# Kernel optimization log

Measured on AMD Instinct MI355X. Metric: run time of the kernel, lower is better.

## Reference

```python
import jax, jax.numpy as jnp
import numpy as np

DIM, NH, WS, SR, CTS = 256, 8, 8, 4, 2
HD = DIM // NH
SCALE = HD ** -0.5

def _linear(x, w, b=None):
    y = x @ w.T
    return y + b if b is not None else y

def _ln(x, g, b, eps=1e-5):
    m = jnp.mean(x, -1, keepdims=True)
    v = jnp.mean((x - m) ** 2, -1, keepdims=True)
    return (x - m) / jnp.sqrt(v + eps) * g + b

def _mlp(x, w1, b1, w2, b2):
    return _linear(jax.nn.gelu(_linear(x, w1, b1), approximate=False), w2, b2)

def _pos_emb_rank3(seq_len, w1, b1, w2):
    # PosEmbMLPSwinv1D with rank=3: coords on cube_root(seq) grid, normalized
    s = int(round(seq_len ** (1.0 / 3.0)))
    c = (jnp.arange(s, dtype=jnp.float32) - s // 2) / (s // 2)
    grid = jnp.stack(jnp.meshgrid(c, c, c, indexing='ij'))      # (3,s,s,s)
    tbl = grid.reshape(3, -1).T                                 # (s^3,3)
    return _linear(jax.nn.relu(_linear(tbl, w1, b1)), w2)[None]  # (1,s^3,dim)

def _rel_bias_3d(ws, w1, b1, w2, n_global):
    # PosEmbMLPSwinv3D: CPB-MLP bias over 3D relative coords, 16*sigmoid, zero-pad for carrier tokens
    r = jnp.arange(-(ws - 1), ws, dtype=jnp.float32)
    tbl = jnp.stack(jnp.meshgrid(r, r, r, indexing='ij'), axis=-1) / (ws - 1)
    tbl = tbl * 8.0
    tbl = jnp.sign(tbl) * jnp.log2(jnp.abs(tbl) + 1.0) / np.log2(8.0)
    table = _linear(jax.nn.relu(_linear(tbl.reshape(-1, 3), w1, b1)), w2)  # ((2ws-1)^3, NH)
    coords = jnp.stack(jnp.meshgrid(jnp.arange(ws), jnp.arange(ws), jnp.arange(ws), indexing='ij'))
    cf = coords.reshape(3, -1)
    rel = (cf[:, :, None] - cf[:, None, :]).transpose(1, 2, 0) + (ws - 1)  # (P,P,3)
    idx = rel[..., 0] * (2 * ws - 1) ** 2 + rel[..., 1] * (2 * ws - 1) + rel[..., 2]
    P = ws ** 3
    bias = table[idx.reshape(-1)].reshape(P, P, NH).transpose(2, 0, 1)
    bias = 16.0 * jax.nn.sigmoid(bias)
    return jnp.pad(bias, ((0, 0), (n_global, 0), (n_global, 0)))[None]  # (1,NH,P+g,P+g)

def _win_attn(x, qkv_w, qkv_b, proj_w, proj_b, bias):
    B, N, C = x.shape
    qkv = _linear(x, qkv_w, qkv_b).reshape(B, N, 3, NH, HD).transpose(2, 0, 3, 1, 4)
    q, k, v = qkv[0], qkv[1], qkv[2]
    attn = jax.nn.softmax(jnp.einsum('bhnd,bhmd->bhnm', q, k) * SCALE + bias, axis=-1)
    out = jnp.einsum('bhnm,bhmd->bhnd', attn, v).transpose(0, 2, 1, 3).reshape(B, N, C)
    return _linear(out, proj_w, proj_b)

def _ct_dewindow(ct, W, H, D, ws):
    bs, _, N = ct.shape
    c = ct.reshape(bs, W // ws, H // ws, D // ws, ws, ws, ws, N)
    c = c.transpose(0, 7, 1, 3, 5, 2, 4, 6).reshape(bs, N, W * H * D)
    return c.transpose(0, 2, 1)

def _ct_window(ct, W, H, D, ws):
    bs, _, N = ct.shape
    c = ct.reshape(bs, H // ws, ws, W // ws, ws, D // ws, ws, N)
    return c.transpose(0, 1, 3, 5, 2, 4, 6, 7)

def setup_inputs() -> dict:
    key = jax.random.key(0)
    ks = jax.random.split(key, 48)
    B0 = 1
    nw = SR ** 3
    def w(k, *s):
        return jax.random.normal(k, s, jnp.float32) * 0.02
    def b(k, *s):
        return jax.random.normal(k, s, jnp.float32) * 0.01
    d4 = 4 * DIM
    return {
        'x': jax.random.normal(ks[0], (B0 * nw, WS ** 3, DIM), jnp.float32),
        'ct': jax.random.normal(ks[1], (B0, (CTS * SR) ** 3, DIM), jnp.float32),
        'pe_w1': w(ks[2], 512, 3), 'pe_b1': b(ks[3], 512), 'pe_w2': w(ks[4], DIM, 512),
        'hpe_w1': w(ks[5], 512, 3), 'hpe_b1': b(ks[6], 512), 'hpe_w2': w(ks[7], DIM, 512),
        'hat_n1_g': jnp.ones((DIM,), jnp.float32), 'hat_n1_b': jnp.zeros((DIM,), jnp.float32),
        'hat_qkv_w': w(ks[8], 3 * DIM, DIM), 'hat_qkv_b': b(ks[9], 3 * DIM),
        'hat_proj_w': w(ks[10], DIM, DIM), 'hat_proj_b': b(ks[11], DIM),
        'hat_cpb_w1': w(ks[12], 512, 3), 'hat_cpb_b1': b(ks[13], 512), 'hat_cpb_w2': w(ks[14], NH, 512),
        'hat_n2_g': jnp.ones((DIM,), jnp.float32), 'hat_n2_b': jnp.zeros((DIM,), jnp.float32),
        'hat_fc1_w': w(ks[15], d4, DIM), 'hat_fc1_b': b(ks[16], d4),
        'hat_fc2_w': w(ks[17], DIM, d4), 'hat_fc2_b': b(ks[18], DIM),
        'n1_g': jnp.ones((DIM,), jnp.float32), 'n1_b': jnp.zeros((DIM,), jnp.float32),
        'qkv_w': w(ks[19], 3 * DIM, DIM), 'qkv_b': b(ks[20], 3 * DIM),
        'proj_w': w(ks[21], DIM, DIM), 'proj_b': b(ks[22], DIM),
        'cpb_w1': w(ks[23], 512, 3), 'cpb_b1': b(ks[24], 512), 'cpb_w2': w(ks[25], NH, 512),
        'n2_g': jnp.ones((DIM,), jnp.float32), 'n2_b': jnp.zeros((DIM,), jnp.float32),
        'fc1_w': w(ks[26], d4, DIM), 'fc1_b': b(ks[27], d4),
        'fc2_w': w(ks[28], DIM, d4), 'fc2_b': b(ks[29], DIM),
    }

def reference(x, ct, pe_w1, pe_b1, pe_w2, hpe_w1, hpe_b1, hpe_w2,
              hat_n1_g, hat_n1_b, hat_qkv_w, hat_qkv_b, hat_proj_w, hat_proj_b,
              hat_cpb_w1, hat_cpb_b1, hat_cpb_w2, hat_n2_g, hat_n2_b,
              hat_fc1_w, hat_fc1_b, hat_fc2_w, hat_fc2_b,
              n1_g, n1_b, qkv_w, qkv_b, proj_w, proj_b,
              cpb_w1, cpb_b1, cpb_w2, n2_g, n2_b, fc1_w, fc1_b, fc2_w, fc2_b):
    Bg, Ng, Hg = ct.shape
    G = CTS * SR  # carrier-token global cube side
    x = x + _pos_emb_rank3(x.shape[1], pe_w1, pe_b1, pe_w2)
    # carrier-token global attention (hierarchical path)
    ct = _ct_dewindow(ct, G, G, G, CTS)
    ct = ct + _pos_emb_rank3(ct.shape[1], hpe_w1, hpe_b1, hpe_w2)
    hat_bias = _rel_bias_3d(G, hat_cpb_w1, hat_cpb_b1, hat_cpb_w2, 0)
    ct = ct + _win_attn(_ln(ct, hat_n1_g, hat_n1_b), hat_qkv_w, hat_qkv_b, hat_proj_w, hat_proj_b, hat_bias)
    ct = ct + _mlp(_ln(ct, hat_n2_g, hat_n2_b), hat_fc1_w, hat_fc1_b, hat_fc2_w, hat_fc2_b)
    ct_w = _ct_window(ct, G, G, G, CTS).reshape(x.shape[0], -1, Hg)
    # windowed attention over [carrier tokens ; window tokens]
    x = jnp.concatenate([ct_w, x], axis=1)
    bias = _rel_bias_3d(WS, cpb_w1, cpb_b1, cpb_w2, CTS ** 3)
    x = x + _win_attn(_ln(x, n1_g, n1_b), qkv_w, qkv_b, proj_w, proj_b, bias)
    x = x + _mlp(_ln(x, n2_g, n2_b), fc1_w, fc1_b, fc2_w, fc2_b)
    split = x.shape[1] - WS ** 3
    ctr, x = x[:, :split], x[:, split:]
    return x, ctr.reshape(Bg, Ng, Hg)
```

## Files before the change

### kernel.cpp

```cpp
#include <hip/hip_runtime.h>
#include <hip/hip_bf16.h>
#include <math.h>

typedef __hip_bfloat16 bf16;

#define SCALE_QK 0.17677669529663687f

__device__ __forceinline__ float b2f(bf16 v){ return __bfloat162float(v); }
__device__ __forceinline__ bf16  f2b(float v){ return __float2bfloat16(v); }
__device__ __forceinline__ short bfs(float x){ bf16 b = f2b(x); short s; __builtin_memcpy(&s, &b, 2); return s; }

struct __align__(16) bf16x8 { bf16 v[8]; };
struct __align__(8)  bf16x4 { bf16 v[4]; };

typedef __attribute__((ext_vector_type(8))) short sh8;
typedef __attribute__((ext_vector_type(4))) short sh4;
typedef __attribute__((ext_vector_type(4))) float f4;

#if defined(__has_builtin)
#if __has_builtin(__builtin_amdgcn_mfma_f32_16x16x16bf16_1k)
#define HAS_MFMA16 1
#else
#define HAS_MFMA16 0
#endif
#else
#define HAS_MFMA16 0
#endif

#if defined(__has_builtin)
#if __has_builtin(__builtin_amdgcn_exp2f)
#define EXP2(x) __builtin_amdgcn_exp2f(x)
#else
#define EXP2(x) exp2f(x)
#endif
#else
#define EXP2(x) exp2f(x)
#endif

__device__ __forceinline__ void gl16(const bf16* g, short* l) {
    __builtin_amdgcn_global_load_lds((const __attribute__((address_space(1))) void*)g,
                                     (__attribute__((address_space(3))) void*)l, 16, 0, 0);
}

__global__ __launch_bounds__(256) void wcvt10_k(const float* s0, const float* s1, const float* s2, const float* s3,
                                                const float* s4, const float* s5, const float* s6, const float* s7,
                                                const float* s8, const float* s9,
                                                bf16* d0, bf16* d1, bf16* d2, bf16* d3, bf16* d4,
                                                bf16* d5, bf16* d6, bf16* d7, bf16* d8, bf16* d9) {
    const int sizes[10] = {196608, 65536, 262144, 262144, 196608, 65536, 262144, 262144, 131072, 131072};
    int which = blockIdx.y;
    const float* s; bf16* d;
    switch (which) {
        case 0: s = s0; d = d0; break;  case 1: s = s1; d = d1; break;
        case 2: s = s2; d = d2; break;  case 3: s = s3; d = d3; break;
        case 4: s = s4; d = d4; break;  case 5: s = s5; d = d5; break;
        case 6: s = s6; d = d6; break;  case 7: s = s7; d = d7; break;
        case 8: s = s8; d = d8; break;  default: s = s9; d = d9; break;
    }
    int i = blockIdx.x * 256 + threadIdx.x;
    if (i < sizes[which]) d[i] = f2b(s[i]);
}

__global__ __launch_bounds__(256) void hidbuild_k(const float* __restrict__ w1a, const float* __restrict__ b1a,
                                                  const float* __restrict__ w1b, const float* __restrict__ b1b,
                                                  bf16* __restrict__ hidA, bf16* __restrict__ hidB) {
    const float* w1 = blockIdx.y ? w1b : w1a;
    const float* b1 = blockIdx.y ? b1b : b1a;
    bf16* hid       = blockIdx.y ? hidB : hidA;
    int t = blockIdx.x, tid = threadIdx.x;
    int i = t >> 6, j = (t >> 3) & 7, k = t & 7;
    float c0 = (i - 4) * 0.25f, c1 = (j - 4) * 0.25f, c2 = (k - 4) * 0.25f;
    #pragma unroll
    for (int rep = 0; rep < 2; rep++) {
        int jj = tid + rep * 256;
        float h = c0 * w1[jj*3+0] + c1 * w1[jj*3+1] + c2 * w1[jj*3+2] + b1[jj];
        hid[(size_t)t * 512 + jj] = f2b(fmaxf(h, 0.f));
    }
}

__device__ __forceinline__ float cpb_coord(int idx) {
    float v = (idx - 7) * (8.0f / 7.0f);
    return copysignf(log2f(fabsf(v) + 1.0f) * (1.0f / 3.0f), v);
}
__global__ __launch_bounds__(512) void cpbtab_k(const float* __restrict__ w1a, const float* __restrict__ b1a,
                                                const float* __restrict__ w2a, float* __restrict__ taba,
                                                const float* __restrict__ w1b, const float* __restrict__ b1b,
                                                const float* __restrict__ w2b, float* __restrict__ tabb) {
    const float* w1 = blockIdx.y ? w1b : w1a;
    const float* b1 = blockIdx.y ? b1b : b1a;
    const float* w2 = blockIdx.y ? w2b : w2a;
    float* tab      = blockIdx.y ? tabb : taba;
    int t = blockIdx.x, tid = threadIdx.x;
    __shared__ float hid[512];
    int i = t / 225, r = t - i * 225, j = r / 15, k = r - j * 15;
    float x0 = cpb_coord(i), x1 = cpb_coord(j), x2 = cpb_coord(k);
    float h = x0 * w1[tid*3+0] + x1 * w1[tid*3+1] + x2 * w1[tid*3+2] + b1[tid];
    hid[tid] = fmaxf(h, 0.f);
    __syncthreads();
    int h8 = tid >> 6, lane = tid & 63;
    float p = 0.f;
    for (int jj = lane; jj < 512; jj += 64) p += hid[jj] * w2[h8*512 + jj];
    for (int off = 32; off; off >>= 1) p += __shfl_down(p, off);
    if (lane == 0) tab[t * 8 + h8] = p;
}

__global__ __launch_bounds__(256) void biasbuild_k(const float* __restrict__ taba, float* __restrict__ biasQa,
                                                   const float* __restrict__ tabb, float* __restrict__ biasQb) {
    const float* tab = blockIdx.y ? tabb : taba;
    float* biasQ     = blockIdx.y ? biasQb : biasQa;
    int idx = blockIdx.x * 256 + threadIdx.x;
    int h = idx >> 18, rem = idx & 262143;
    int q = rem >> 9, k = rem & 511;
    int qx = q >> 6, qy = (q >> 3) & 7, qz = q & 7;
    int kx = k >> 6, ky = (k >> 3) & 7, kz = k & 7;
    int tidx = ((qx - kx + 7) * 15 + (qy - ky + 7)) * 15 + (qz - kz + 7);
    float v = tab[tidx * 8 + h];
    float b = 16.f / (1.f + __expf(-v));
    biasQ[idx] = (b - 24.0f) * 1.4426950408889634f;
}

__global__ __launch_bounds__(256) void ct0ln_k(const float* __restrict__ ct_in,
                                               const float* __restrict__ hpe,
                                               const float* __restrict__ g,
                                               const float* __restrict__ b,
                                               float* __restrict__ ct0,
                                               bf16* __restrict__ lnout) {
    int u = blockIdx.x, c = threadIdx.x;
    int a = u >> 7, cc = (u >> 5) & 3, e = (u >> 4) & 1, bb = (u >> 2) & 3, d = (u >> 1) & 1, f = u & 1;
    int t = a * 128 + bb * 32 + cc * 8 + d * 4 + e * 2 + f;
    float x = ct_in[(size_t)t * 256 + c] + hpe[(size_t)u * 256 + c];
    ct0[(size_t)u * 256 + c] = x;
    float s = x, s2 = x * x;
    for (int off = 32; off; off >>= 1) { s += __shfl_down(s, off); s2 += __shfl_down(s2, off); }
    __shared__ float red[8];
    int wid = c >> 6, lane = c & 63;
    if (lane == 0) { red[wid] = s; red[wid + 4] = s2; }
    __syncthreads();
    if (c == 0) { red[0] = red[0] + red[1] + red[2] + red[3]; red[4] = red[4] + red[5] + red[6] + red[7]; }
    __syncthreads();
    float mean = red[0] * (1.f / 256.f);
    float var  = fmaxf(red[4] * (1.f / 256.f) - mean * mean, 0.f);
    float rstd = rsqrtf(var + 1e-5f);
    lnout[(size_t)u * 256 + c] = f2b((x - mean) * rstd * g[c] + b[c]);
}

__global__ __launch_bounds__(256) void ln_k(const float* __restrict__ in,
                                            const float* __restrict__ g,
                                            const float* __restrict__ b,
                                            bf16* __restrict__ out) {
    int row = blockIdx.x, c = threadIdx.x;
    float x = in[(size_t)row * 256 + c];
    float s = x, s2 = x * x;
    for (int off = 32; off; off >>= 1) { s += __shfl_down(s, off); s2 += __shfl_down(s2, off); }
    __shared__ float red[8];
    int wid = c >> 6, lane = c & 63;
    if (lane == 0) { red[wid] = s; red[wid + 4] = s2; }
    __syncthreads();
    if (c == 0) { red[0] = red[0] + red[1] + red[2] + red[3]; red[4] = red[4] + red[5] + red[6] + red[7]; }
    __syncthreads();
    float mean = red[0] * (1.f / 256.f);
    float var  = fmaxf(red[4] * (1.f / 256.f) - mean * mean, 0.f);
    float rstd = rsqrtf(var + 1e-5f);
    out[(size_t)row * 256 + c] = f2b((x - mean) * rstd * g[c] + b[c]);
}

template <int MODE>
__global__ __launch_bounds__(256) void gemm_k(const bf16* __restrict__ A,
                                              const bf16* __restrict__ W,
                                              const float* __restrict__ bias,
                                              int M, int N, int K,
                                              float* __restrict__ res,
                                              bf16* __restrict__ outb) {
    __shared__ short As[2][128 * 32];
    __shared__ short Ws[2][128 * 32];
    int m0 = blockIdx.y * 128, n0 = blockIdx.x * 128;
    int tid = threadIdx.x;
    int lane = tid & 63, wave = tid >> 6;
    int quad = lane >> 4, m16 = lane & 15;
    int wm = (wave & 1) * 64, wn = (wave >> 1) * 64;
    int arow = tid >> 2, acol = (tid & 3) * 8;

    const bf16* Ab = A + (size_t)(m0 + arow) * K + acol;
    const bf16* A2 = Ab + (size_t)64 * K;
    const bf16* Wb = W + (size_t)(n0 + arow) * K + acol;
    const bf16* W2 = Wb + (size_t)64 * K;

    f4 acc[4][4];
    #pragma unroll
    for (int i = 0; i < 4; i++)
        #pragma unroll
        for (int j = 0; j < 4; j++) acc[i][j] = (f4){0.f, 0.f, 0.f, 0.f};

    gl16(Ab, &As[0][tid * 8]);
    gl16(A2, &As[0][2048 + tid * 8]);
    gl16(Wb, &Ws[0][tid * 8]);
    gl16(W2, &Ws[0][2048 + tid * 8]);

    int cur = 0;
    for (int k0 = 0; k0 < K; k0 += 32) {
        int nxt = cur ^ 1;
        if (k0 + 32 < K) {
            gl16(Ab + k0 + 32, &As[nxt][tid * 8]);
            gl16(A2 + k0 + 32, &As[nxt][2048 + tid * 8]);
            gl16(Wb + k0 + 32, &Ws[nxt][tid * 8]);
            gl16(W2 + k0 + 32, &Ws[nxt][2048 + tid * 8]);
            asm volatile("s_waitcnt vmcnt(4)" ::: "memory");
        } else {
            asm volatile("s_waitcnt vmcnt(0)" ::: "memory");
        }
        __builtin_amdgcn_s_barrier();
        sh8 af[4], bf[4];
        #pragma unroll
        for (int mi = 0; mi < 4; mi++)
            af[mi] = *reinterpret_cast<const sh8*>(&As[cur][(wm + mi * 16 + m16) * 32 + quad * 8]);
        #pragma unroll
        for (int ni = 0; ni < 4; ni++)
            bf[ni] = *reinterpret_cast<const sh8*>(&Ws[cur][(wn + ni * 16 + m16) * 32 + quad * 8]);
        #pragma unroll
        for (int mi = 0; mi < 4; mi++)
            #pragma unroll
            for (int ni = 0; ni < 4; ni++)
                acc[mi][ni] = __builtin_amdgcn_mfma_f32_16x16x32_bf16(af[mi], bf[ni], acc[mi][ni], 0, 0, 0);
        __builtin_amdgcn_s_barrier();
        cur = nxt;
    }
    (void)M;

    #pragma unroll
    for (int mi = 0; mi < 4; mi++) {
        #pragma unroll
        for (int r = 0; r < 4; r++) {
            int gm = m0 + wm + mi * 16 + quad * 4 + r;
            #pragma unroll
            for (int ni = 0; ni < 4; ni++) {
                int gn = n0 + wn + ni * 16 + m16;
                float v = acc[mi][ni][r];
                if constexpr (MODE != 3) v += bias[gn];
                if constexpr (MODE == 2)      res[(size_t)gm * N + gn] += v;
                else if constexpr (MODE == 3) res[(size_t)gm * N + gn] = v;
                else if constexpr (MODE == 1) outb[(size_t)gm * N + gn] = f2b(0.5f * v * (1.0f + erff(v * 0.70710678118654752f)));
                else                          outb[(size_t)gm * N + gn] = f2b(v);
            }
        }
    }
}

__global__ __launch_bounds__(512) void gemmln_k(const bf16* __restrict__ A,
                                                const bf16* __restrict__ W,
                                                const float* __restrict__ bias,
                                                float* __restrict__ xcat,
                                                const float* __restrict__ g,
                                                const float* __restrict__ b,
                                                bf16* __restrict__ outb) {
    __shared__ short As[2][128 * 32];
    __shared__ short Ws[2][256 * 32];
    __shared__ float redS[128 * 4];
    __shared__ float redQ[128 * 4];
    __shared__ float stat[128 * 2];
    int m0 = blockIdx.x * 128;
    int tid = threadIdx.x;
    int lane = tid & 63, wave = tid >> 6;
    int quad = lane >> 4, m16 = lane & 15;
    int wm = (wave >> 2) * 64, wn = (wave & 3) * 64;
    int arow = tid >> 2, acol = (tid & 3) * 8;

    const bf16* Ab = A + (size_t)(m0 + arow) * 256 + acol;
    const bf16* Wb = W + (size_t)arow * 256 + acol;
    const bf16* W2 = Wb + (size_t)128 * 256;

    f4 acc[4][4];
    #pragma unroll
    for (int i = 0; i < 4; i++)
        #pragma unroll
        for (int j = 0; j < 4; j++) acc[i][j] = (f4){0.f, 0.f, 0.f, 0.f};

    gl16(Ab, &As[0][tid * 8]);
    gl16(Wb, &Ws[0][tid * 8]);
    gl16(W2, &Ws[0][4096 + tid * 8]);

    int cur = 0;
    for (int k0 = 0; k0 < 256; k0 += 32) {
        int nxt = cur ^ 1;
        if (k0 + 32 < 256) {
            gl16(Ab + k0 + 32, &As[nxt][tid * 8]);
            gl16(Wb + k0 + 32, &Ws[nxt][tid * 8]);
            gl16(W2 + k0 + 32, &Ws[nxt][4096 + tid * 8]);
            asm volatile("s_waitcnt vmcnt(3)" ::: "memory");
        } else {
            asm volatile("s_waitcnt vmcnt(0)" ::: "memory");
        }
        __builtin_amdgcn_s_barrier();
        sh8 af[4], bf[4];
        #pragma unroll
        for (int mi = 0; mi < 4; mi++)
            af[mi] = *reinterpret_cast<const sh8*>(&As[cur][(wm + mi * 16 + m16) * 32 + quad * 8]);
        #pragma unroll
        for (int ni = 0; ni < 4; ni++)
            bf[ni] = *reinterpret_cast<const sh8*>(&Ws[cur][(wn + ni * 16 + m16) * 32 + quad * 8]);
        #pragma unroll
        for (int mi = 0; mi < 4; mi++)
            #pragma unroll
            for (int ni = 0; ni < 4; ni++)
                acc[mi][ni] = __builtin_amdgcn_mfma_f32_16x16x32_bf16(af[mi], bf[ni], acc[mi][ni], 0, 0, 0);
        __builtin_amdgcn_s_barrier();
        cur = nxt;
    }

    #pragma unroll
    for (int mi = 0; mi < 4; mi++) {
        #pragma unroll
        for (int r = 0; r < 4; r++) {
            int lr = wm + mi * 16 + quad * 4 + r;
            int gm = m0 + lr;
            float ps = 0.f, pq = 0.f;
            #pragma unroll
            for (int ni = 0; ni < 4; ni++) {
                int gc = wn + ni * 16 + m16;
                float v = acc[mi][ni][r] + bias[gc] + xcat[(size_t)gm * 256 + gc];
                acc[mi][ni][r] = v;
                ps += v; pq += v * v;
            }
            ps += __shfl_xor(ps, 1); pq += __shfl_xor(pq, 1);
            ps += __shfl_xor(ps, 2); pq += __shfl_xor(pq, 2);
            ps += __shfl_xor(ps, 4); pq += __shfl_xor(pq, 4);
            ps += __shfl_xor(ps, 8); pq += __shfl_xor(pq, 8);
            if (m16 == 0) { redS[lr * 4 + (wave & 3)] = ps; redQ[lr * 4 + (wave & 3)] = pq; }
        }
    }
    __syncthreads();
    if (tid < 128) {
        float s = redS[tid * 4] + redS[tid * 4 + 1] + redS[tid * 4 + 2] + redS[tid * 4 + 3];
        float q = redQ[tid * 4] + redQ[tid * 4 + 1] + redQ[tid * 4 + 2] + redQ[tid * 4 + 3];
        float mean = s * (1.f / 256.f);
        float var  = fmaxf(q * (1.f / 256.f) - mean * mean, 0.f);
        stat[tid * 2]     = mean;
        stat[tid * 2 + 1] = rsqrtf(var + 1e-5f);
    }
    __syncthreads();
    #pragma unroll
    for (int mi = 0; mi < 4; mi++) {
        #pragma unroll
        for (int r = 0; r < 4; r++) {
            int lr = wm + mi * 16 + quad * 4 + r;
            int gm = m0 + lr;
            float mean = stat[lr * 2], rstd = stat[lr * 2 + 1];
            #pragma unroll
            for (int ni = 0; ni < 4; ni++) {
                int gc = wn + ni * 16 + m16;
                float v = acc[mi][ni][r];
                xcat[(size_t)gm * 256 + gc] = v;
                outb[(size_t)gm * 256 + gc] = f2b((v - mean) * rstd * g[gc] + b[gc]);
            }
        }
    }
}

__global__ __launch_bounds__(256) void gemmsplit_k(const bf16* __restrict__ A,
                                                   const bf16* __restrict__ W,
                                                   const float* __restrict__ bias,
                                                   int K,
                                                   const float* __restrict__ res,
                                                   float* __restrict__ out) {
    __shared__ short As[2][128 * 32];
    __shared__ short Ws[2][128 * 32];
    int m0 = blockIdx.y * 128, n0 = blockIdx.x * 128;
    int tid = threadIdx.x;
    int lane = tid & 63, wave = tid >> 6;
    int quad = lane >> 4, m16 = lane & 15;
    int wm = (wave & 1) * 64, wn = (wave >> 1) * 64;
    int arow = tid >> 2, acol = (tid & 3) * 8;

    const bf16* Ab = A + (size_t)(m0 + arow) * K + acol;
    const bf16* A2 = Ab + (size_t)64 * K;
    const bf16* Wb = W + (size_t)(n0 + arow) * K + acol;
    const bf16* W2 = Wb + (size_t)64 * K;

    f4 acc[4][4];
    #pragma unroll
    for (int i = 0; i < 4; i++)
        #pragma unroll
        for (int j = 0; j < 4; j++) acc[i][j] = (f4){0.f, 0.f, 0.f, 0.f};

    gl16(Ab, &As[0][tid * 8]);
    gl16(A2, &As[0][2048 + tid * 8]);
    gl16(Wb, &Ws[0][tid * 8]);
    gl16(W2, &Ws[0][2048 + tid * 8]);

    int cur = 0;
    for (int k0 = 0; k0 < K; k0 += 32) {
        int nxt = cur ^ 1;
        if (k0 + 32 < K) {
            gl16(Ab + k0 + 32, &As[nxt][tid * 8]);
            gl16(A2 + k0 + 32, &As[nxt][2048 + tid * 8]);
            gl16(Wb + k0 + 32, &Ws[nxt][tid * 8]);
            gl16(W2 + k0 + 32, &Ws[nxt][2048 + tid * 8]);
            asm volatile("s_waitcnt vmcnt(4)" ::: "memory");
        } else {
            asm volatile("s_waitcnt vmcnt(0)" ::: "memory");
        }
        __builtin_amdgcn_s_barrier();
        sh8 af[4], bf[4];
        #pragma unroll
        for (int mi = 0; mi < 4; mi++)
            af[mi] = *reinterpret_cast<const sh8*>(&As[cur][(wm + mi * 16 + m16) * 32 + quad * 8]);
        #pragma unroll
        for (int ni = 0; ni < 4; ni++)
            bf[ni] = *reinterpret_cast<const sh8*>(&Ws[cur][(wn + ni * 16 + m16) * 32 + quad * 8]);
        #pragma unroll
        for (int mi = 0; mi < 4; mi++)
            #pragma unroll
            for (int ni = 0; ni < 4; ni++)
                acc[mi][ni] = __builtin_amdgcn_mfma_f32_16x16x32_bf16(af[mi], bf[ni], acc[mi][ni], 0, 0, 0);
        __builtin_amdgcn_s_barrier();
        cur = nxt;
    }

    #pragma unroll
    for (int mi = 0; mi < 4; mi++) {
        #pragma unroll
        for (int r = 0; r < 4; r++) {
            int gm = m0 + wm + mi * 16 + quad * 4 + r;
            int w = gm / 520, p = gm - w * 520;
            size_t drow = (p >= 8) ? (size_t)(w * 512 + p - 8) : (size_t)(32768 + w * 8 + p);
            #pragma unroll
            for (int ni = 0; ni < 4; ni++) {
                int gn = n0 + wn + ni * 16 + m16;
                float v = acc[mi][ni][r] + bias[gn] + res[(size_t)gm * 256 + gn];
                out[drow * 256 + gn] = v;
            }
        }
    }
}

#define VSTR 548
#define SC2   0.25503575360579045f
#define CNB  (-34.62468098133512f)
#define NEGB (-1.0e30f)
__device__ __forceinline__ f4 bias_ld(const float* brow, bool vq, int tg, int N, int glob) {
    if (tg >= N) return (f4){NEGB, NEGB, NEGB, NEGB};
    if (vq && tg >= glob) return *reinterpret_cast<const f4*>(brow + tg);
    return (f4){CNB, CNB, CNB, CNB};
}
__global__ __launch_bounds__(512) void flash_k(const bf16* __restrict__ qkv,
                                               const float* __restrict__ biasQ,
                                               bf16* __restrict__ out,
                                               int N, int glob) {
    int wh = blockIdx.x, w = wh >> 3, h = wh & 7;
    int qs = blockIdx.y;
    int tid = threadIdx.x;
    int lane = tid & 63, wave = tid >> 6;
    int quad = lane >> 4, qcol = lane & 15;
    const int NT32 = (N + 31) & ~31;

    __shared__ __align__(16) char smem[32 * VSTR * 2];
    bf16* Vt = reinterpret_cast<bf16*>(smem);
#if !HAS_MFMA16
    __shared__ float Ps[8][16 * 17];
#endif

    for (int i = tid; i < NT32 * 4; i += 512) {
        int tok = i >> 2, seg = i & 3;
        if (tok < N) {
            const bf16* vp = qkv + ((size_t)(w * N + tok)) * 768 + 512 + h * 32 + seg * 8;
            bf16x8 vv = *reinterpret_cast<const bf16x8*>(vp);
            #pragma unroll
            for (int e = 0; e < 8; e++) Vt[(seg * 8 + e) * VSTR + tok] = vv.v[e];
        } else {
            bf16 z = f2b(0.f);
            #pragma unroll
            for (int e = 0; e < 8; e++) Vt[(seg * 8 + e) * VSTR + tok] = z;
        }
    }
    __syncthreads();

    const bf16* qbase = qkv + ((size_t)w * N) * 768 + h * 32;
    const bf16* kbase = qbase + 256;
    int nqt = (N + 15) >> 4, nkt = NT32 >> 5;
    int nfull = nqt >> 1;

    if (qs < 2) {
        int u = wave + 8 * qs;
        if (u < nfull) {
            int qA = u * 32 + qcol;
            int qB = qA + 16;
            sh8 qfA = *reinterpret_cast<const sh8*>(qbase + (size_t)qA * 768 + quad * 8);
            sh8 qfB = *reinterpret_cast<const sh8*>(qbase + (size_t)qB * 768 + quad * 8);
            f4 O0A = {0.f,0.f,0.f,0.f}, O1A = {0.f,0.f,0.f,0.f};
            f4 O0B = {0.f,0.f,0.f,0.f}, O1B = {0.f,0.f,0.f,0.f};
            float lA = 0.f, lB = 0.f;
            bool vA = (qA >= glob);
            bool vB = (qB >= glob);
            const float* browA = biasQ + (((size_t)h << 9) + (size_t)(vA ? (qA - glob) : 0)) * 512 - glob;
            const float* browB = biasQ + (((size_t)h << 9) + (size_t)(vB ? (qB - glob) : 0)) * 512 - glob;

            sh8 kf0, kf1;
            f4 nb0A, nb1A, nb0B, nb1B;
            {
                int k0 = qcol, k1 = 16 + qcol;
                kf0 = *reinterpret_cast<const sh8*>(kbase + (size_t)((k0 < N) ? k0 : (N - 1)) * 768 + quad * 8);
                kf1 = *reinterpret_cast<const sh8*>(kbase + (size_t)((k1 < N) ? k1 : (N - 1)) * 768 + quad * 8);
                int tg0 = quad * 4, tg1 = 16 + quad * 4;
                nb0A = bias_ld(browA, vA, tg0, N, glob);
                nb1A = bias_ld(browA, vA, tg1, N, glob);
                nb0B = bias_ld(browB, vB, tg0, N, glob);
                nb1B = bias_ld(browB, vB, tg1, N, glob);
            }

            for (int kt = 0; kt < nkt; kt++) {
                int bt = kt * 32;
                sh8 c0 = kf0, c1 = kf1;
                f4 bb0A = nb0A, bb1A = nb1A, bb0B = nb0B, bb1B = nb1B;
                if (kt + 1 < nkt) {
                    int btn = bt + 32;
                    int n0 = btn + qcol, n1 = btn + 16 + qcol;
                    kf0 = *reinterpret_cast<const sh8*>(kbase + (size_t)((n0 < N) ? n0 : (N - 1)) * 768 + quad * 8);
                    kf1 = *reinterpret_cast<const sh8*>(kbase + (size_t)((n1 < N) ? n1 : (N - 1)) * 768 + quad * 8);
                    int tg0n = btn + quad * 4, tg1n = btn + 16 + quad * 4;
                    nb0A = bias_ld(browA, vA, tg0n, N, glob);
                    nb1A = bias_ld(browA, vA, tg1n, N, glob);
                    nb0B = bias_ld(browB, vB, tg0n, N, glob);
                    nb1B = bias_ld(browB, vB, tg1n, N, glob);
                }
                f4 z = {0.f, 0.f, 0.f, 0.f};
                f4 s0A = __builtin_amdgcn_mfma_f32_16x16x32_bf16(c0, qfA, z, 0, 0, 0);
                f4 s1A = __builtin_amdgcn_mfma_f32_16x16x32_bf16(c1, qfA, z, 0, 0, 0);
                f4 s0B = __builtin_amdgcn_mfma_f32_16x16x32_bf16(c0, qfB, z, 0, 0, 0);
                f4 s1B = __builtin_amdgcn_mfma_f32_16x16x32_bf16(c1, qfB, z, 0, 0, 0);

                float pA[8], pB[8];
                #pragma unroll
                for (int r = 0; r < 4; r++) {
                    pA[r]     = EXP2(fmaf(s0A[r], SC2, bb0A[r]));
                    pA[4 + r] = EXP2(fmaf(s1A[r], SC2, bb1A[r]));
                    pB[r]     = EXP2(fmaf(s0B[r], SC2, bb0B[r]));
                    pB[4 + r] = EXP2(fmaf(s1B[r], SC2, bb1B[r]));
                }
                #pragma unroll
                for (int r = 0; r < 8; r++) { lA += pA[r]; lB += pB[r]; }

#if HAS_MFMA16
                sh4 v00 = *reinterpret_cast<const sh4*>(&Vt[qcol * VSTR + bt + quad * 4]);
                sh4 v10 = *reinterpret_cast<const sh4*>(&Vt[qcol * VSTR + bt + 16 + quad * 4]);
                sh4 v01 = *reinterpret_cast<const sh4*>(&Vt[(qcol + 16) * VSTR + bt + quad * 4]);
                sh4 v11 = *reinterpret_cast<const sh4*>(&Vt[(qcol + 16) * VSTR + bt + 16 + quad * 4]);
                sh4 pf0A, pf1A, pf0B, pf1B;
                #pragma unroll
                for (int r = 0; r < 4; r++) {
                    pf0A[r] = bfs(pA[r]); pf1A[r] = bfs(pA[4 + r]);
                    pf0B[r] = bfs(pB[r]); pf1B[r] = bfs(pB[4 + r]);
                }
                O0A = __builtin_amdgcn_mfma_f32_16x16x16bf16_1k(v00, pf0A, O0A, 0, 0, 0);
                O0A = __builtin_amdgcn_mfma_f32_16x16x16bf16_1k(v10, pf1A, O0A, 0, 0, 0);
                O1A = __builtin_amdgcn_mfma_f32_16x16x16bf16_1k(v01, pf0A, O1A, 0, 0, 0);
                O1A = __builtin_amdgcn_mfma_f32_16x16x16bf16_1k(v11, pf1A, O1A, 0, 0, 0);
                O0B = __builtin_amdgcn_mfma_f32_16x16x16bf16_1k(v00, pf0B, O0B, 0, 0, 0);
                O0B = __builtin_amdgcn_mfma_f32_16x16x16bf16_1k(v10, pf1B, O0B, 0, 0, 0);
                O1B = __builtin_amdgcn_mfma_f32_16x16x16bf16_1k(v01, pf0B, O1B, 0, 0, 0);
                O1B = __builtin_amdgcn_mfma_f32_16x16x16bf16_1k(v11, pf1B, O1B, 0, 0, 0);
#else
                for (int t = 0; t < 2; t++) {
                    const float* ph = t ? pB : pA;
                    for (int half = 0; half < 2; half++) {
                        #pragma unroll
                        for (int r = 0; r < 4; r++) Ps[wave][(quad * 4 + r) * 17 + qcol] = ph[half * 4 + r];
                        __builtin_amdgcn_wave_barrier();
                        sh8 pbig, va, vb;
                        #pragma unroll
                        for (int j = 0; j < 8; j++) {
                            int tl = quad * 8 + j;
                            float pv = (quad < 2) ? Ps[wave][tl * 17 + qcol] : 0.f;
                            pbig[j] = bfs(pv);
                            bf16 a0 = (quad < 2) ? Vt[qcol * VSTR + bt + half * 16 + tl] : f2b(0.f);
                            bf16 a1 = (quad < 2) ? Vt[(qcol + 16) * VSTR + bt + half * 16 + tl] : f2b(0.f);
                            short t0, t1;
                            __builtin_memcpy(&t0, &a0, 2); __builtin_memcpy(&t1, &a1, 2);
                            va[j] = t0; vb[j] = t1;
                        }
                        if (t == 0) {
                            O0A = __builtin_amdgcn_mfma_f32_16x16x32_bf16(va, pbig, O0A, 0, 0, 0);
                            O1A = __builtin_amdgcn_mfma_f32_16x16x32_bf16(vb, pbig, O1A, 0, 0, 0);
                        } else {
                            O0B = __builtin_amdgcn_mfma_f32_16x16x32_bf16(va, pbig, O0B, 0, 0, 0);
                            O1B = __builtin_amdgcn_mfma_f32_16x16x32_bf16(vb, pbig, O1B, 0, 0, 0);
                        }
                        __builtin_amdgcn_wave_barrier();
                    }
                }
#endif
            }

            lA += __shfl_xor(lA, 16); lA += __shfl_xor(lA, 32);
            lB += __shfl_xor(lB, 16); lB += __shfl_xor(lB, 32);
            float rlA = 1.f / lA, rlB = 1.f / lB;
            {
                bf16x4 o0, o1;
                #pragma unroll
                for (int r = 0; r < 4; r++) { o0.v[r] = f2b(O0A[r] * rlA); o1.v[r] = f2b(O1A[r] * rlA); }
                bf16* op = out + ((size_t)(w * N + qA)) * 256 + h * 32 + quad * 4;
                *reinterpret_cast<bf16x4*>(op)      = o0;
                *reinterpret_cast<bf16x4*>(op + 16) = o1;
            }
            {
                bf16x4 o0, o1;
                #pragma unroll
                for (int r = 0; r < 4; r++) { o0.v[r] = f2b(O0B[r] * rlB); o1.v[r] = f2b(O1B[r] * rlB); }
                bf16* op = out + ((size_t)(w * N + qB)) * 256 + h * 32 + quad * 4;
                *reinterpret_cast<bf16x4*>(op)      = o0;
                *reinterpret_cast<bf16x4*>(op + 16) = o1;
            }
        }
    } else {
        int rt = nqt - 1;
        int qA = rt * 16 + qcol;
        int qrA = (qA < N) ? qA : (N - 1);
        sh8 qfA = *reinterpret_cast<const sh8*>(qbase + (size_t)qrA * 768 + quad * 8);
        f4 O0 = {0.f,0.f,0.f,0.f}, O1 = {0.f,0.f,0.f,0.f};
        float l = 0.f;
        bool vA = (qA >= glob) && (qA < N);
        const float* browA = biasQ + (((size_t)h << 9) + (size_t)(vA ? (qA - glob) : 0)) * 512 - glob;

        for (int kt = wave; kt < nkt; kt += 8) {
            int bt = kt * 32;
            int k0 = bt + qcol, k1 = bt + 16 + qcol;
            sh8 c0 = *reinterpret_cast<const sh8*>(kbase + (size_t)((k0 < N) ? k0 : (N - 1)) * 768 + quad * 8);
            sh8 c1 = *reinterpret_cast<const sh8*>(kbase + (size_t)((k1 < N) ? k1 : (N - 1)) * 768 + quad * 8);
            f4 z = {0.f, 0.f, 0.f, 0.f};
            f4 s0 = __builtin_amdgcn_mfma_f32_16x16x32_bf16(c0, qfA, z, 0, 0, 0);
            f4 s1 = __builtin_amdgcn_mfma_f32_16x16x32_bf16(c1, qfA, z, 0, 0, 0);

            int tg0 = bt + quad * 4, tg1 = bt + 16 + quad * 4;
            f4 bb0 = bias_ld(browA, vA, tg0, N, glob);
            f4 bb1 = bias_ld(browA, vA, tg1, N, glob);

            float p[8];
            #pragma unroll
            for (int r = 0; r < 4; r++) {
                p[r]     = EXP2(fmaf(s0[r], SC2, bb0[r]));
                p[4 + r] = EXP2(fmaf(s1[r], SC2, bb1[r]));
            }
            #pragma unroll
            for (int r = 0; r < 8; r++) l += p[r];

#if HAS_MFMA16
            sh4 v00 = *reinterpret_cast<const sh4*>(&Vt[qcol * VSTR + bt + quad * 4]);
            sh4 v10 = *reinterpret_cast<const sh4*>(&Vt[qcol * VSTR + bt + 16 + quad * 4]);
            sh4 v01 = *reinterpret_cast<const sh4*>(&Vt[(qcol + 16) * VSTR + bt + quad * 4]);
            sh4 v11 = *reinterpret_cast<const sh4*>(&Vt[(qcol + 16) * VSTR + bt + 16 + quad * 4]);
            sh4 pf0, pf1;
            #pragma unroll
            for (int r = 0; r < 4; r++) { pf0[r] = bfs(p[r]); pf1[r] = bfs(p[4 + r]); }
            O0 = __builtin_amdgcn_mfma_f32_16x16x16bf16_1k(v00, pf0, O0, 0, 0, 0);
            O0 = __builtin_amdgcn_mfma_f32_16x16x16bf16_1k(v10, pf1, O0, 0, 0, 0);
            O1 = __builtin_amdgcn_mfma_f32_16x16x16bf16_1k(v01, pf0, O1, 0, 0, 0);
            O1 = __builtin_amdgcn_mfma_f32_16x16x16bf16_1k(v11, pf1, O1, 0, 0, 0);
#else
            for (int half = 0; half < 2; half++) {
                #pragma unroll
                for (int r = 0; r < 4; r++) Ps[wave][(quad * 4 + r) * 17 + qcol] = p[half * 4 + r];
                __builtin_amdgcn_wave_barrier();
                sh8 pbig, va, vb;
                #pragma unroll
                for (int j = 0; j < 8; j++) {
                    int tl = quad * 8 + j;
                    float pv = (quad < 2) ? Ps[wave][tl * 17 + qcol] : 0.f;
                    pbig[j] = bfs(pv);
                    bf16 a0 = (quad < 2) ? Vt[qcol * VSTR + bt + half * 16 + tl] : f2b(0.f);
                    bf16 a1 = (quad < 2) ? Vt[(qcol + 16) * VSTR + bt + half * 16 + tl] : f2b(0.f);
                    short t0, t1;
                    __builtin_memcpy(&t0, &a0, 2); __builtin_memcpy(&t1, &a1, 2);
                    va[j] = t0; vb[j] = t1;
                }
                O0 = __builtin_amdgcn_mfma_f32_16x16x32_bf16(va, pbig, O0, 0, 0, 0);
                O1 = __builtin_amdgcn_mfma_f32_16x16x32_bf16(vb, pbig, O1, 0, 0, 0);
                __builtin_amdgcn_wave_barrier();
            }
#endif
        }

        __syncthreads();
        float (*red)[64][9] = reinterpret_cast<float (*)[64][9]>(smem);
        #pragma unroll
        for (int r = 0; r < 4; r++) { red[wave][lane][r] = O0[r]; red[wave][lane][4 + r] = O1[r]; }
        red[wave][lane][8] = l;
        __syncthreads();

        if (wave == 0) {
            f4 O0s = {0.f,0.f,0.f,0.f}, O1s = {0.f,0.f,0.f,0.f};
            float ls = 0.f;
            for (int v = 0; v < 8; v++) {
                #pragma unroll
                for (int r = 0; r < 4; r++) { O0s[r] += red[v][lane][r]; O1s[r] += red[v][lane][4 + r]; }
                ls += red[v][lane][8];
            }
            ls += __shfl_xor(ls, 16); ls += __shfl_xor(ls, 32);
            float rl = 1.f / ls;
            if (qA < N) {
                bf16x4 o0, o1;
                #pragma unroll
                for (int r = 0; r < 4; r++) { o0.v[r] = f2b(O0s[r] * rl); o1.v[r] = f2b(O1s[r] * rl); }
                bf16* op = out + ((size_t)(w * N + qA)) * 256 + h * 32 + quad * 4;
                *reinterpret_cast<bf16x4*>(op)      = o0;
                *reinterpret_cast<bf16x4*>(op + 16) = o1;
            }
        }
    }
}

__global__ __launch_bounds__(256) void xcatln_k(const float* __restrict__ x_in,
                                                const float* __restrict__ pe,
                                                const float* __restrict__ ct2,
                                                const float* __restrict__ g,
                                                const float* __restrict__ b,
                                                float* __restrict__ xcat,
                                                bf16* __restrict__ xln) {
    int row = blockIdx.x, w = row / 520, p = row - w * 520, c = threadIdx.x;
    float v;
    if (p < 8) {
        int P = w >> 4, Q = (w >> 2) & 3, R = w & 3;
        int S = p >> 2, T = (p >> 1) & 1, U = p & 1;
        int t = P * 128 + S * 64 + Q * 16 + T * 8 + R * 2 + U;
        v = ct2[(size_t)t * 256 + c];
    } else {
        int t = p - 8;
        v = x_in[((size_t)w * 512 + t) * 256 + c] + pe[(size_t)t * 256 + c];
    }
    xcat[(size_t)row * 256 + c] = v;
    float s = v, s2 = v * v;
    for (int off = 32; off; off >>= 1) { s += __shfl_down(s, off); s2 += __shfl_down(s2, off); }
    __shared__ float red[8];
    int wid = c >> 6, lane = c & 63;
    if (lane == 0) { red[wid] = s; red[wid + 4] = s2; }
    __syncthreads();
    if (c == 0) { red[0] = red[0] + red[1] + red[2] + red[3]; red[4] = red[4] + red[5] + red[6] + red[7]; }
    __syncthreads();
    float mean = red[0] * (1.f / 256.f);
    float var  = fmaxf(red[4] * (1.f / 256.f) - mean * mean, 0.f);
    float rstd = rsqrtf(var + 1e-5f);
    xln[(size_t)row * 256 + c] = f2b((v - mean) * rstd * g[c] + b[c]);
}

__global__ __launch_bounds__(256) void xcatbuild_k(const float* __restrict__ x_in,
                                                   const float* __restrict__ pe,
                                                   const float* __restrict__ ct2,
                                                   float* __restrict__ xcat) {
    int row = blockIdx.x, w = row / 520, p = row - w * 520, c = threadIdx.x;
    float v;
    if (p < 8) {
        int P = w >> 4, Q = (w >> 2) & 3, R = w & 3;
        int S = p >> 2, T = (p >> 1) & 1, U = p & 1;
        int t = P * 128 + S * 64 + Q * 16 + T * 8 + R * 2 + U;
        v = ct2[(size_t)t * 256 + c];
    } else {
        int t = p - 8;
        v = x_in[((size_t)w * 512 + t) * 256 + c] + pe[(size_t)t * 256 + c];
    }
    xcat[(size_t)row * 256 + c] = v;
}

__global__ __launch_bounds__(256) void outbuild_k(const float* __restrict__ xcat,
                                                  float* __restrict__ out) {
    int row = blockIdx.x, w = row / 520, p = row - w * 520, c = threadIdx.x;
    float v = xcat[(size_t)row * 256 + c];
    if (p >= 8) out[((size_t)(w * 512) + (p - 8)) * 256 + c] = v;
    else        out[(size_t)8388608 + ((size_t)(w * 8) + p) * 256 + c] = v;
}

extern "C" void kernel_launch(void* const* d_in, const int* in_sizes, int n_in,
                              void* d_out, int out_size, void* d_ws, size_t ws_size,
                              hipStream_t stream) {
    const float* x          = (const float*)d_in[0];
    const float* ct         = (const float*)d_in[1];
    const float* pe_w1      = (const float*)d_in[2];
    const float* pe_b1      = (const float*)d_in[3];
    const float* pe_w2      = (const float*)d_in[4];
    const float* hpe_w1     = (const float*)d_in[5];
    const float* hpe_b1     = (const float*)d_in[6];
    const float* hpe_w2     = (const float*)d_in[7];
    const float* hat_n1_g   = (const float*)d_in[8];
    const float* hat_n1_b   = (const float*)d_in[9];
    const float* hat_qkv_w  = (const float*)d_in[10];
    const float* hat_qkv_b  = (const float*)d_in[11];
    const float* hat_proj_w = (const float*)d_in[12];
    const float* hat_proj_b = (const float*)d_in[13];
    const float* hat_cpb_w1 = (const float*)d_in[14];
    const float* hat_cpb_b1 = (const float*)d_in[15];
    const float* hat_cpb_w2 = (const float*)d_in[16];
    const float* hat_n2_g   = (const float*)d_in[17];
    const float* hat_n2_b   = (const float*)d_in[18];
    const float* hat_fc1_w  = (const float*)d_in[19];
    const float* hat_fc1_b  = (const float*)d_in[20];
    const float* hat_fc2_w  = (const float*)d_in[21];
    const float* hat_fc2_b  = (const float*)d_in[22];
    const float* n1_g       = (const float*)d_in[23];
    const float* n1_b       = (const float*)d_in[24];
    const float* qkv_w      = (const float*)d_in[25];
    const float* qkv_b      = (const float*)d_in[26];
    const float* proj_w     = (const float*)d_in[27];
    const float* proj_b     = (const float*)d_in[28];
    const float* cpb_w1     = (const float*)d_in[29];
    const float* cpb_b1     = (const float*)d_in[30];
    const float* cpb_w2     = (const float*)d_in[31];
    const float* n2_g       = (const float*)d_in[32];
    const float* n2_b       = (const float*)d_in[33];
    const float* fc1_w      = (const float*)d_in[34];
    const float* fc1_b      = (const float*)d_in[35];
    const float* fc2_w      = (const float*)d_in[36];
    const float* fc2_b      = (const float*)d_in[37];
    (void)in_sizes; (void)n_in; (void)out_size;

    char* base = (char*)d_ws;
    size_t off = 0;
    auto alloc = [&](size_t bytes) -> void* {
        void* p = base + off;
        off += (bytes + 255) & ~(size_t)255;
        return p;
    };
    float* pe        = (float*)alloc(512 * 256 * 4);
    float* hpe       = (float*)alloc(512 * 256 * 4);
    float* tab_hat   = (float*)alloc(3375 * 8 * 4);
    float* tab2      = (float*)alloc(3375 * 8 * 4);
    float* biasQ2    = (float*)alloc((size_t)8 * 512 * 512 * 4);
    float* ct0       = (float*)alloc(512 * 256 * 4);
    bf16* wb_hqkv  = (bf16*)alloc(768 * 256 * 2);
    bf16* wb_hproj = (bf16*)alloc(256 * 256 * 2);
    bf16* wb_hfc1  = (bf16*)alloc(1024 * 256 * 2);
    bf16* wb_hfc2  = (bf16*)alloc(256 * 1024 * 2);
    bf16* wb_qkv   = (bf16*)alloc(768 * 256 * 2);
    bf16* wb_proj  = (bf16*)alloc(256 * 256 * 2);
    bf16* wb_fc1   = (bf16*)alloc(1024 * 256 * 2);
    bf16* wb_fc2   = (bf16*)alloc(256 * 1024 * 2);
    bf16* wb_pew2  = (bf16*)alloc(256 * 512 * 2);
    bf16* wb_hpew2 = (bf16*)alloc(256 * 512 * 2);
    size_t zstart = off;
    bf16*  hidA      = (bf16*)alloc(512 * 512 * 2);
    bf16*  hidB      = (bf16*)alloc(512 * 512 * 2);
    off = zstart;
    float* biasQ_hat = (float*)alloc((size_t)8 * 512 * 512 * 4);
    bf16*  hct_ln    = (bf16*)alloc(512 * 256 * 2);
    bf16*  hqkv      = (bf16*)alloc(512 * 768 * 2);
    bf16*  hat_attn  = (bf16*)alloc(512 * 256 * 2);
    bf16*  hat_hid   = (bf16*)alloc(512 * 1024 * 2);
    off = zstart;
    float* xcat      = (float*)alloc((size_t)64 * 520 * 256 * 4);
    const int S     = (ws_size >= (size_t)150 * 1024 * 1024) ? 1 : 4;
    const int rows  = 33280 / S;
    const int wins  = 64 / S;
    bf16*  xln_b     = (bf16*)alloc((size_t)rows * 256 * 2);
    char*  region_qa = (char*)alloc((size_t)rows * 1024 * 2);
    bf16*  qkv_b_    = (bf16*)region_qa;
    bf16*  attn_b    = (bf16*)(region_qa + (size_t)rows * 768 * 2);
    bf16*  hidden    = (bf16*)region_qa;

    wcvt10_k<<<dim3(1024, 10), 256, 0, stream>>>(hat_qkv_w, hat_proj_w, hat_fc1_w, hat_fc2_w,
                                                 qkv_w, proj_w, fc1_w, fc2_w, pe_w2, hpe_w2,
                                                 wb_hqkv, wb_hproj, wb_hfc1, wb_hfc2,
                                                 wb_qkv, wb_proj, wb_fc1, wb_fc2, wb_pew2, wb_hpew2);

    hidbuild_k<<<dim3(512, 2), 256, 0, stream>>>(pe_w1, pe_b1, hpe_w1, hpe_b1, hidA, hidB);
    gemm_k<3><<<dim3(2, 4), 256, 0, stream>>>(hidA, wb_pew2,  nullptr, 512, 256, 512, pe,  nullptr);
    gemm_k<3><<<dim3(2, 4), 256, 0, stream>>>(hidB, wb_hpew2, nullptr, 512, 256, 512, hpe, nullptr);

    cpbtab_k<<<dim3(3375, 2), 512, 0, stream>>>(hat_cpb_w1, hat_cpb_b1, hat_cpb_w2, tab_hat,
                                                cpb_w1, cpb_b1, cpb_w2, tab2);
    biasbuild_k<<<dim3(8192, 2), 256, 0, stream>>>(tab_hat, biasQ_hat, tab2, biasQ2);

    ct0ln_k<<<512, 256, 0, stream>>>(ct, hpe, hat_n1_g, hat_n1_b, ct0, hct_ln);
    gemm_k<0><<<dim3(6, 4), 256, 0, stream>>>(hct_ln, wb_hqkv, hat_qkv_b, 512, 768, 256, nullptr, hqkv);
    flash_k<<<dim3(8, 2), 512, 0, stream>>>(hqkv, biasQ_hat, hat_attn, 512, 0);
    gemmln_k<<<4, 512, 0, stream>>>(hat_attn, wb_hproj, hat_proj_b, ct0, hat_n2_g, hat_n2_b, hct_ln);
    gemm_k<1><<<dim3(8, 4), 256, 0, stream>>>(hct_ln, wb_hfc1, hat_fc1_b, 512, 1024, 256, nullptr, hat_hid);
    gemm_k<2><<<dim3(2, 4), 256, 0, stream>>>(hat_hid, wb_hfc2, hat_fc2_b, 512, 256, 1024, ct0, nullptr);

    if (S == 1) {
        xcatln_k<<<33280, 256, 0, stream>>>(x, pe, ct0, n1_g, n1_b, xcat, xln_b);
        gemm_k<0><<<dim3(6, 260), 256, 0, stream>>>(xln_b, wb_qkv, qkv_b, 33280, 768, 256, nullptr, qkv_b_);
        flash_k<<<dim3(512, 3), 512, 0, stream>>>(qkv_b_, biasQ2, attn_b, 520, 8);
        gemmln_k<<<260, 512, 0, stream>>>(attn_b, wb_proj, proj_b, xcat, n2_g, n2_b, xln_b);
        gemm_k<1><<<dim3(8, 260), 256, 0, stream>>>(xln_b, wb_fc1, fc1_b, 33280, 1024, 256, nullptr, hidden);
        gemmsplit_k<<<dim3(2, 260), 256, 0, stream>>>(hidden, wb_fc2, fc2_b, 1024, xcat, (float*)d_out);
    } else {
        xcatbuild_k<<<33280, 256, 0, stream>>>(x, pe, ct0, xcat);
        for (int s = 0; s < S; s++) {
            float* xc = xcat + (size_t)s * rows * 256;
            ln_k<<<rows, 256, 0, stream>>>(xc, n1_g, n1_b, xln_b);
            gemm_k<0><<<dim3(6, rows / 128), 256, 0, stream>>>(xln_b, wb_qkv, qkv_b, rows, 768, 256, nullptr, qkv_b_);
            flash_k<<<dim3(wins * 8, 3), 512, 0, stream>>>(qkv_b_, biasQ2, attn_b, 520, 8);
            gemm_k<2><<<dim3(2, rows / 128), 256, 0, stream>>>(attn_b, wb_proj, proj_b, rows, 256, 256, xc, nullptr);
        }
        for (int s = 0; s < S; s++) {
            float* xc = xcat + (size_t)s * rows * 256;
            ln_k<<<rows, 256, 0, stream>>>(xc, n2_g, n2_b, xln_b);
            gemm_k<1><<<dim3(8, rows / 128), 256, 0, stream>>>(xln_b, wb_fc1, fc1_b, rows, 1024, 256, nullptr, hidden);
            gemm_k<2><<<dim3(2, rows / 128), 256, 0, stream>>>(hidden, wb_fc2, fc2_b, rows, 256, 1024, xc, nullptr);
        }
        outbuild_k<<<33280, 256, 0, stream>>>(xcat, (float*)d_out);
    }
}
```

Measured before the change: 577.9 us.

## Gather relative position bias from compact table inside flash attention

Result: faster. 532.1 us (-7.9%).

```diff
diff --git a/kernel.cpp b/kernel.cpp
--- a/kernel.cpp
+++ b/kernel.cpp
@@ -101,22 +101,10 @@
     float p = 0.f;
     for (int jj = lane; jj < 512; jj += 64) p += hid[jj] * w2[h8*512 + jj];
     for (int off = 32; off; off >>= 1) p += __shfl_down(p, off);
-    if (lane == 0) tab[t * 8 + h8] = p;
-}
-
-__global__ __launch_bounds__(256) void biasbuild_k(const float* __restrict__ taba, float* __restrict__ biasQa,
-                                                   const float* __restrict__ tabb, float* __restrict__ biasQb) {
-    const float* tab = blockIdx.y ? tabb : taba;
-    float* biasQ     = blockIdx.y ? biasQb : biasQa;
-    int idx = blockIdx.x * 256 + threadIdx.x;
-    int h = idx >> 18, rem = idx & 262143;
-    int q = rem >> 9, k = rem & 511;
-    int qx = q >> 6, qy = (q >> 3) & 7, qz = q & 7;
-    int kx = k >> 6, ky = (k >> 3) & 7, kz = k & 7;
-    int tidx = ((qx - kx + 7) * 15 + (qy - ky + 7)) * 15 + (qz - kz + 7);
-    float v = tab[tidx * 8 + h];
-    float b = 16.f / (1.f + __expf(-v));
-    biasQ[idx] = (b - 24.0f) * 1.4426950408889634f;
+    if (lane == 0) {
+        float bsig = 16.f / (1.f + __expf(-p));
+        tab[h8 * 3375 + t] = (bsig - 24.0f) * 1.4426950408889634f;
+    }
 }
 
 __global__ __launch_bounds__(256) void ct0ln_k(const float* __restrict__ ct_in,
@@ -436,13 +424,23 @@
 #define SC2   0.25503575360579045f
 #define CNB  (-34.62468098133512f)
 #define NEGB (-1.0e30f)
-__device__ __forceinline__ f4 bias_ld(const float* brow, bool vq, int tg, int N, int glob) {
+__device__ __forceinline__ int cpb_kidx(int kl) {
+    return (kl >> 6) * 225 + ((kl >> 3) & 7) * 15 + (kl & 7);
+}
+__device__ __forceinline__ int cpb_qconst(int ql) {
+    return ((ql >> 6) + 7) * 225 + (((ql >> 3) & 7) + 7) * 15 + ((ql & 7) + 7);
+}
+__device__ __forceinline__ f4 bias_tab(const float* __restrict__ tabh, bool vq, int qc,
+                                       int tg, int kidx, int N, int glob) {
     if (tg >= N) return (f4){NEGB, NEGB, NEGB, NEGB};
-    if (vq && tg >= glob) return *reinterpret_cast<const f4*>(brow + tg);
+    if (vq && tg >= glob) {
+        int t0 = qc - kidx;
+        return (f4){tabh[t0], tabh[t0 - 1], tabh[t0 - 2], tabh[t0 - 3]};
+    }
     return (f4){CNB, CNB, CNB, CNB};
 }
 __global__ __launch_bounds__(512) void flash_k(const bf16* __restrict__ qkv,
-                                               const float* __restrict__ biasQ,
+                                               const float* __restrict__ tab,
                                                bf16* __restrict__ out,
                                                int N, int glob) {
     int wh = blockIdx.x, w = wh >> 3, h = wh & 7;
@@ -451,6 +449,7 @@
     int lane = tid & 63, wave = tid >> 6;
     int quad = lane >> 4, qcol = lane & 15;
     const int NT32 = (N + 31) & ~31;
+    const float* __restrict__ tabh = tab + h * 3375;
 
     __shared__ __align__(16) char smem[32 * VSTR * 2];
     bf16* Vt = reinterpret_cast<bf16*>(smem);
@@ -490,42 +489,37 @@
             float lA = 0.f, lB = 0.f;
             bool vA = (qA >= glob);
             bool vB = (qB >= glob);
-            const float* browA = biasQ + (((size_t)h << 9) + (size_t)(vA ? (qA - glob) : 0)) * 512 - glob;
-            const float* browB = biasQ + (((size_t)h << 9) + (size_t)(vB ? (qB - glob) : 0)) * 512 - glob;
+            int qcA = vA ? cpb_qconst(qA - glob) : 0;
+            int qcB = vB ? cpb_qconst(qB - glob) : 0;
 
             sh8 kf0, kf1;
-            f4 nb0A, nb1A, nb0B, nb1B;
             {
                 int k0 = qcol, k1 = 16 + qcol;
                 kf0 = *reinterpret_cast<const sh8*>(kbase + (size_t)((k0 < N) ? k0 : (N - 1)) * 768 + quad * 8);
                 kf1 = *reinterpret_cast<const sh8*>(kbase + (size_t)((k1 < N) ? k1 : (N - 1)) * 768 + quad * 8);
-                int tg0 = quad * 4, tg1 = 16 + quad * 4;
-                nb0A = bias_ld(browA, vA, tg0, N, glob);
-                nb1A = bias_ld(browA, vA, tg1, N, glob);
-                nb0B = bias_ld(browB, vB, tg0, N, glob);
-                nb1B = bias_ld(browB, vB, tg1, N, glob);
             }
 
             for (int kt = 0; kt < nkt; kt++) {
                 int bt = kt * 32;
                 sh8 c0 = kf0, c1 = kf1;
-                f4 bb0A = nb0A, bb1A = nb1A, bb0B = nb0B, bb1B = nb1B;
                 if (kt + 1 < nkt) {
-                    int btn = bt + 32;
-                    int n0 = btn + qcol, n1 = btn + 16 + qcol;
+                    int n0 = bt + 32 + qcol, n1 = bt + 48 + qcol;
                     kf0 = *reinterpret_cast<const sh8*>(kbase + (size_t)((n0 < N) ? n0 : (N - 1)) * 768 + quad * 8);
                     kf1 = *reinterpret_cast<const sh8*>(kbase + (size_t)((n1 < N) ? n1 : (N - 1)) * 768 + quad * 8);
-                    int tg0n = btn + quad * 4, tg1n = btn + 16 + quad * 4;
-                    nb0A = bias_ld(browA, vA, tg0n, N, glob);
-                    nb1A = bias_ld(browA, vA, tg1n, N, glob);
-                    nb0B = bias_ld(browB, vB, tg0n, N, glob);
-                    nb1B = bias_ld(browB, vB, tg1n, N, glob);
                 }
                 f4 z = {0.f, 0.f, 0.f, 0.f};
                 f4 s0A = __builtin_amdgcn_mfma_f32_16x16x32_bf16(c0, qfA, z, 0, 0, 0);
                 f4 s1A = __builtin_amdgcn_mfma_f32_16x16x32_bf16(c1, qfA, z, 0, 0, 0);
                 f4 s0B = __builtin_amdgcn_mfma_f32_16x16x32_bf16(c0, qfB, z, 0, 0, 0);
                 f4 s1B = __builtin_amdgcn_mfma_f32_16x16x32_bf16(c1, qfB, z, 0, 0, 0);
+
+                int tg0 = bt + quad * 4, tg1 = tg0 + 16;
+                int kidx0 = cpb_kidx(tg0 - glob);
+                int kidx1 = cpb_kidx(tg1 - glob);
+                f4 bb0A = bias_tab(tabh, vA, qcA, tg0, kidx0, N, glob);
+                f4 bb1A = bias_tab(tabh, vA, qcA, tg1, kidx1, N, glob);
+                f4 bb0B = bias_tab(tabh, vB, qcB, tg0, kidx0, N, glob);
+                f4 bb1B = bias_tab(tabh, vB, qcB, tg1, kidx1, N, glob);
 
                 float pA[8], pB[8];
                 #pragma unroll
@@ -617,7 +611,7 @@
         f4 O0 = {0.f,0.f,0.f,0.f}, O1 = {0.f,0.f,0.f,0.f};
         float l = 0.f;
         bool vA = (qA >= glob) && (qA < N);
-        const float* browA = biasQ + (((size_t)h << 9) + (size_t)(vA ? (qA - glob) : 0)) * 512 - glob;
+        int qcA = vA ? cpb_qconst(qA - glob) : 0;
 
         for (int kt = wave; kt < nkt; kt += 8) {
             int bt = kt * 32;
@@ -628,9 +622,11 @@
             f4 s0 = __builtin_amdgcn_mfma_f32_16x16x32_bf16(c0, qfA, z, 0, 0, 0);
             f4 s1 = __builtin_amdgcn_mfma_f32_16x16x32_bf16(c1, qfA, z, 0, 0, 0);
 
-            int tg0 = bt + quad * 4, tg1 = bt + 16 + quad * 4;
-            f4 bb0 = bias_ld(browA, vA, tg0, N, glob);
-            f4 bb1 = bias_ld(browA, vA, tg1, N, glob);
+            int tg0 = bt + quad * 4, tg1 = tg0 + 16;
+            int kidx0 = cpb_kidx(tg0 - glob);
+            int kidx1 = cpb_kidx(tg1 - glob);
+            f4 bb0 = bias_tab(tabh, vA, qcA, tg0, kidx0, N, glob);
+            f4 bb1 = bias_tab(tabh, vA, qcA, tg1, kidx1, N, glob);
 
             float p[8];
             #pragma unroll
@@ -817,9 +813,8 @@
     };
     float* pe        = (float*)alloc(512 * 256 * 4);
     float* hpe       = (float*)alloc(512 * 256 * 4);
-    float* tab_hat   = (float*)alloc(3375 * 8 * 4);
-    float* tab2      = (float*)alloc(3375 * 8 * 4);
-    float* biasQ2    = (float*)alloc((size_t)8 * 512 * 512 * 4);
+    float* tab_hat   = (float*)alloc(8 * 3375 * 4);
+    float* tab2      = (float*)alloc(8 * 3375 * 4);
     float* ct0       = (float*)alloc(512 * 256 * 4);
     bf16* wb_hqkv  = (bf16*)alloc(768 * 256 * 2);
     bf16* wb_hproj = (bf16*)alloc(256 * 256 * 2);
@@ -835,7 +830,6 @@
     bf16*  hidA      = (bf16*)alloc(512 * 512 * 2);
     bf16*  hidB      = (bf16*)alloc(512 * 512 * 2);
     off = zstart;
-    float* biasQ_hat = (float*)alloc((size_t)8 * 512 * 512 * 4);
     bf16*  hct_ln    = (bf16*)alloc(512 * 256 * 2);
     bf16*  hqkv      = (bf16*)alloc(512 * 768 * 2);
     bf16*  hat_attn  = (bf16*)alloc(512 * 256 * 2);
@@ -862,11 +856,10 @@
 
     cpbtab_k<<<dim3(3375, 2), 512, 0, stream>>>(hat_cpb_w1, hat_cpb_b1, hat_cpb_w2, tab_hat,
                                                 cpb_w1, cpb_b1, cpb_w2, tab2);
-    biasbuild_k<<<dim3(8192, 2), 256, 0, stream>>>(tab_hat, biasQ_hat, tab2, biasQ2);
 
     ct0ln_k<<<512, 256, 0, stream>>>(ct, hpe, hat_n1_g, hat_n1_b, ct0, hct_ln);
     gemm_k<0><<<dim3(6, 4), 256, 0, stream>>>(hct_ln, wb_hqkv, hat_qkv_b, 512, 768, 256, nullptr, hqkv);
-    flash_k<<<dim3(8, 2), 512, 0, stream>>>(hqkv, biasQ_hat, hat_attn, 512, 0);
+    flash_k<<<dim3(8, 2), 512, 0, stream>>>(hqkv, tab_hat, hat_attn, 512, 0);
     gemmln_k<<<4, 512, 0, stream>>>(hat_attn, wb_hproj, hat_proj_b, ct0, hat_n2_g, hat_n2_b, hct_ln);
     gemm_k<1><<<dim3(8, 4), 256, 0, stream>>>(hct_ln, wb_hfc1, hat_fc1_b, 512, 1024, 256, nullptr, hat_hid);
     gemm_k<2><<<dim3(2, 4), 256, 0, stream>>>(hat_hid, wb_hfc2, hat_fc2_b, 512, 256, 1024, ct0, nullptr);
@@ -874,7 +867,7 @@
     if (S == 1) {
         xcatln_k<<<33280, 256, 0, stream>>>(x, pe, ct0, n1_g, n1_b, xcat, xln_b);
         gemm_k<0><<<dim3(6, 260), 256, 0, stream>>>(xln_b, wb_qkv, qkv_b, 33280, 768, 256, nullptr, qkv_b_);
-        flash_k<<<dim3(512, 3), 512, 0, stream>>>(qkv_b_, biasQ2, attn_b, 520, 8);
+        flash_k<<<dim3(512, 3), 512, 0, stream>>>(qkv_b_, tab2, attn_b, 520, 8);
         gemmln_k<<<260, 512, 0, stream>>>(attn_b, wb_proj, proj_b, xcat, n2_g, n2_b, xln_b);
         gemm_k<1><<<dim3(8, 260), 256, 0, stream>>>(xln_b, wb_fc1, fc1_b, 33280, 1024, 256, nullptr, hidden);
         gemmsplit_k<<<dim3(2, 260), 256, 0, stream>>>(hidden, wb_fc2, fc2_b, 1024, xcat, (float*)d_out);
@@ -884,7 +877,7 @@
             float* xc = xcat + (size_t)s * rows * 256;
             ln_k<<<rows, 256, 0, stream>>>(xc, n1_g, n1_b, xln_b);
             gemm_k<0><<<dim3(6, rows / 128), 256, 0, stream>>>(xln_b, wb_qkv, qkv_b, rows, 768, 256, nullptr, qkv_b_);
-            flash_k<<<dim3(wins * 8, 3), 512, 0, stream>>>(qkv_b_, biasQ2, attn_b, 520, 8);
+            flash_k<<<dim3(wins * 8, 3), 512, 0, stream>>>(qkv_b_, tab2, attn_b, 520, 8);
             gemm_k<2><<<dim3(2, rows / 128), 256, 0, stream>>>(attn_b, wb_proj, proj_b, rows, 256, 256, xc, nullptr);
         }
         for (int s = 0; s < S; s++) {
```
